# Kernel tuning notes

Hardware: AMD Instinct MI355X
Metric: run time of the kernel (lower is better)

Reference implementation:

```python
import jax, jax.numpy as jnp
import numpy as np

B, S, H = 1, 4096, 2048
NH, NKV, HD = 16, 4, 128  # query heads, kv heads, head_dim
THETA = 1000000.0
NEG = -1e9


def setup_inputs() -> dict:
    key = jax.random.key(0)
    ks = jax.random.split(key, 5)
    hidden_states = jax.random.normal(ks[0], (B, S, H), jnp.float32) * 0.02
    Wq = jax.random.normal(ks[1], (H, NH * HD), jnp.float32) * 0.02
    Wk = jax.random.normal(ks[2], (H, NKV * HD), jnp.float32) * 0.02
    Wv = jax.random.normal(ks[3], (H, NKV * HD), jnp.float32) * 0.02
    Wo = jax.random.normal(ks[4], (H, H), jnp.float32) * 0.02
    # additive causal mask [B,1,S,S]
    causal = jnp.tril(jnp.ones((S, S), bool))
    attention_mask = jnp.where(causal, 0.0, NEG).astype(jnp.float32)[None, None]
    position_ids = jnp.arange(S, dtype=jnp.int32)[None]
    return dict(hidden_states=hidden_states, Wq=Wq, Wk=Wk, Wv=Wv, Wo=Wo,
                attention_mask=attention_mask, position_ids=position_ids)


def _rotate_half(x):
    return jnp.concatenate([-x[..., HD // 2:], x[..., :HD // 2]], axis=-1)


def reference(hidden_states, Wq, Wk, Wv, Wo, attention_mask, position_ids):
    # projections -> [B, heads, S, HD]
    q = (hidden_states @ Wq).reshape(B, S, NH, HD).transpose(0, 2, 1, 3)
    k = (hidden_states @ Wk).reshape(B, S, NKV, HD).transpose(0, 2, 1, 3)
    v = (hidden_states @ Wv).reshape(B, S, NKV, HD).transpose(0, 2, 1, 3)

    # RoPE (HF style: freqs duplicated across halves, rotate_half)
    inv_freq = 1.0 / (THETA ** (jnp.arange(0, HD, 2, dtype=jnp.float32) / HD))
    freqs = position_ids.astype(jnp.float32)[..., None] * inv_freq  # [B,S,HD/2]
    emb = jnp.concatenate([freqs, freqs], axis=-1)                  # [B,S,HD]
    cos = jnp.cos(emb)[:, None].astype(q.dtype)                     # [B,1,S,HD]
    sin = jnp.sin(emb)[:, None].astype(q.dtype)
    q = q * cos + _rotate_half(q) * sin
    k = k * cos + _rotate_half(k) * sin

    # GQA: repeat each kv head consecutively (matches torch repeat_kv)
    rep = NH // NKV
    k = jnp.repeat(k, rep, axis=1)
    v = jnp.repeat(v, rep, axis=1)

    scale = 1.0 / jnp.sqrt(jnp.float32(HD))
    scores = jnp.einsum('bhqd,bhkd->bhqk', q, k) * scale + attention_mask
    attn = jax.nn.softmax(scores.astype(jnp.float32), axis=-1).astype(q.dtype)
    out = jnp.einsum('bhqk,bhkd->bhqd', attn, v)  # [B,NH,S,HD]
    out = out.transpose(0, 2, 1, 3).reshape(B, S, H)
    return out @ Wo
```

## Files before the change

kernel.cpp:

```cpp
#include <hip/hip_runtime.h>
#include <stdint.h>

typedef uint16_t u16;
typedef __bf16  bf16x8 __attribute__((ext_vector_type(8)));
typedef float   f32x4  __attribute__((ext_vector_type(4)));
typedef float   f32x16 __attribute__((ext_vector_type(16)));
typedef uint16_t u16x8 __attribute__((ext_vector_type(8), may_alias));
typedef uint32_t u32x4 __attribute__((ext_vector_type(4)));

typedef const __attribute__((address_space(1))) void* gas_p;
typedef __attribute__((address_space(3))) void* las_p;

#define SCALE2 0.1275430214486847f

__device__ __forceinline__ void load_lds16(const void* g, void* l) {
    __builtin_amdgcn_global_load_lds((gas_p)g, (las_p)l, 16, 0, 0);
}

__device__ __forceinline__ u16 f2bf(float f) {
    uint32_t u = __builtin_bit_cast(uint32_t, f);
    u += 0x7FFFu + ((u >> 16) & 1u);
    return (u16)(u >> 16);
}
__device__ __forceinline__ float bf2f(u16 h) {
    uint32_t u = ((uint32_t)h) << 16;
    return __builtin_bit_cast(float, u);
}
__device__ __forceinline__ bf16x8 ld_frag(const u16* p) {
    u16x8 t = *(const u16x8*)p;
    return __builtin_bit_cast(bf16x8, t);
}
__device__ __forceinline__ uint32_t cvt_pk_bf16(float lo, float hi) {
    uint32_t r;
    asm("v_cvt_pk_bf16_f32 %0, %1, %2" : "=v"(r) : "v"(lo), "v"(hi));
    return r;
}
__device__ __forceinline__ void plane32_swap(uint32_t& a, uint32_t& b) {
    asm("v_permlane32_swap_b32 %0, %1" : "+v"(a), "+v"(b));
}

__global__ __launch_bounds__(256) void prep(const float* __restrict__ hidden,
                                            u16* __restrict__ Hb,
                                            const float* __restrict__ Wq,
                                            u16* __restrict__ WqT,
                                            const float* __restrict__ Wk,
                                            const float* __restrict__ Wv,
                                            u16* __restrict__ WkvT) {
    __shared__ u16 tile[64][65];
    const int bid = blockIdx.x;
    const int tx  = threadIdx.x;
    if (bid < 4096) {
        int i = bid * 256 + tx;
        const float* p = hidden + (size_t)i * 8;
        u16x8 o;
#pragma unroll
        for (int j = 0; j < 8; j++) o[j] = f2bf(p[j]);
        *(u16x8*)(Hb + (size_t)i * 8) = o;
        return;
    }
    const float* in;
    u16* out;
    int R, C, bx, by;
    if (bid < 5120)      { int l = bid - 4096; in = Wq; out = WqT;            R = 2048; C = 2048; bx = l & 31; by = l >> 5; }
    else if (bid < 5376) { int l = bid - 5120; in = Wk; out = WkvT;           R = 2048; C = 512;  bx = l & 7;  by = l >> 3; }
    else                 { int l = bid - 5376; in = Wv; out = WkvT + 1048576; R = 2048; C = 512;  bx = l & 7;  by = l >> 3; }
    const int bc = bx * 64, br = by * 64;
#pragma unroll
    for (int i = 0; i < 16; i++) {
        int idx = tx + i * 256;
        int r = idx >> 6, c = idx & 63;
        tile[r][c] = f2bf(in[(size_t)(br + r) * C + bc + c]);
    }
    __syncthreads();
#pragma unroll
    for (int i = 0; i < 16; i++) {
        int idx = tx + i * 256;
        int r = idx >> 6, c = idx & 63;
        out[(size_t)(bc + r) * R + br + c] = tile[c][r];
    }
}

__global__ __launch_bounds__(256) void mid(u16* __restrict__ Q,
                                           u16* __restrict__ KV,
                                           const float* __restrict__ Wo,
                                           u16* __restrict__ WoT,
                                           u16* __restrict__ VT) {
    __shared__ u16 tile[64][65];
    const int bid = blockIdx.x;
    const int tx  = threadIdx.x;
    if (bid < 20480) {
        int g = bid * 256 + tx;
        int d = g & 63;
        int row = g >> 6;
        int s = row / 20;
        int hh = row - s * 20;
        u16* buf = (hh < 16) ? (Q + (size_t)s * 2048 + hh * 128)
                             : (KV + (size_t)s * 1024 + (hh - 16) * 128);
        float p = (float)s;
        float angle = p * exp2f((float)d * (-19.931568569324174f / 64.0f));
        float sc = (hh < 16) ? SCALE2 : 1.0f;
        float c = cosf(angle) * sc, sn = sinf(angle) * sc;
        float x0 = bf2f(buf[d]), x1 = bf2f(buf[d + 64]);
        buf[d]      = f2bf(x0 * c - x1 * sn);
        buf[d + 64] = f2bf(x1 * c + x0 * sn);
        return;
    }
    if (bid < 21504) {
        int l = bid - 20480;
        int bc = (l & 31) * 64, br = (l >> 5) * 64;
#pragma unroll
        for (int i = 0; i < 16; i++) {
            int idx = tx + i * 256;
            int r = idx >> 6, c = idx & 63;
            tile[r][c] = f2bf(Wo[(size_t)(br + r) * 2048 + bc + c]);
        }
        __syncthreads();
#pragma unroll
        for (int i = 0; i < 16; i++) {
            int idx = tx + i * 256;
            int r = idx >> 6, c = idx & 63;
            WoT[(size_t)(bc + r) * 2048 + br + c] = tile[c][r];
        }
        return;
    }
    {
        int l = bid - 21504;
        int bc = (l & 7) * 64, br = (l >> 3) * 64;
#pragma unroll
        for (int i = 0; i < 16; i++) {
            int idx = tx + i * 256;
            int r = idx >> 6, c = idx & 63;
            tile[r][c] = KV[(size_t)(br + r) * 1024 + 512 + bc + c];
        }
        __syncthreads();
#pragma unroll
        for (int i = 0; i < 16; i++) {
            int idx = tx + i * 256;
            int r = idx >> 6, c = idx & 63;
            VT[(size_t)(bc + r) * 4096 + br + c] = tile[c][r];
        }
    }
}

#define TM 128
#define TN 128

__global__ __launch_bounds__(256) void gemm_qkv(const u16* __restrict__ A,
                                                const u16* __restrict__ WqT,
                                                const u16* __restrict__ WkvT,
                                                u16* __restrict__ Qb,
                                                u16* __restrict__ KVb) {
    __shared__ u16 As[128 * 64];
    __shared__ u16 Bs[128 * 64];
    const int K = 2048;
    const int tid  = threadIdx.x;
    const int wave = tid >> 6;
    const int lane = tid & 63;
    const int l15  = lane & 15;
    const int quad = lane >> 4;
    const int m0 = blockIdx.y * TM;
    const int n0 = blockIdx.x * TN;
    const u16* Bt;
    u16* C;
    int ldC, cbase;
    if (n0 < 2048) { Bt = WqT + (size_t)n0 * K;          C = Qb;  ldC = 2048; cbase = n0; }
    else           { Bt = WkvT + (size_t)(n0 - 2048) * K; C = KVb; ldC = 1024; cbase = n0 - 2048; }
    const int wm = (wave >> 1) * 64;
    const int wn = (wave & 1) * 64;

    f32x4 acc[4][4] = {};

    const int srow = tid >> 3;
    const int swc  = ((tid & 7) ^ (srow & 7)) * 8;
    const u16* Ap[4];
    const u16* Bp[4];
#pragma unroll
    for (int r = 0; r < 4; r++) {
        Ap[r] = A  + (size_t)(m0 + srow + r * 32) * K + swc;
        Bp[r] = Bt + (size_t)(srow + r * 32) * K + swc;
    }
    u16* AsD = As + wave * 512;
    u16* BsD = Bs + wave * 512;

    for (int k0 = 0; k0 < K; k0 += 64) {
#pragma unroll
        for (int r = 0; r < 4; r++) load_lds16(Ap[r] + k0, AsD + r * 2048);
#pragma unroll
        for (int r = 0; r < 4; r++) load_lds16(Bp[r] + k0, BsD + r * 2048);
        __syncthreads();
        bf16x8 af[2][4], bfr[2][4];
        const int sx = (l15 & 7) << 3;
#pragma unroll
        for (int kk = 0; kk < 2; kk++)
#pragma unroll
            for (int i = 0; i < 4; i++) {
                af[kk][i]  = ld_frag(&As[((wm + i * 16 + l15) * 64 + kk * 32 + quad * 8) ^ sx]);
                bfr[kk][i] = ld_frag(&Bs[((wn + i * 16 + l15) * 64 + kk * 32 + quad * 8) ^ sx]);
            }
#pragma unroll
        for (int kk = 0; kk < 2; kk++)
#pragma unroll
            for (int i = 0; i < 4; i++)
#pragma unroll
                for (int j = 0; j < 4; j++)
                    acc[i][j] = __builtin_amdgcn_mfma_f32_16x16x32_bf16(af[kk][i], bfr[kk][j], acc[i][j], 0, 0, 0);
        __syncthreads();
    }
#pragma unroll
    for (int i = 0; i < 4; i++)
#pragma unroll
        for (int j = 0; j < 4; j++)
#pragma unroll
            for (int r = 0; r < 4; r++) {
                int row = m0 + wm + i * 16 + quad * 4 + r;
                int col = cbase + wn + j * 16 + l15;
                C[(size_t)row * ldC + col] = f2bf(acc[i][j][r]);
            }
}

template <bool F32OUT>
__global__ __launch_bounds__(256) void gemm_bt(const u16* __restrict__ A,
                                               const u16* __restrict__ Bt,
                                               void* __restrict__ Cp,
                                               int M, int N, int K) {
    __shared__ u16 As[128 * 64];
    __shared__ u16 Bs[128 * 64];
    const int tid  = threadIdx.x;
    const int wave = tid >> 6;
    const int lane = tid & 63;
    const int l15  = lane & 15;
    const int quad = lane >> 4;
    const int m0 = blockIdx.y * TM;
    const int n0 = blockIdx.x * TN;
    const int wm = (wave >> 1) * 64;
    const int wn = (wave & 1) * 64;

    f32x4 acc[4][4] = {};

    const int srow = tid >> 3;
    const int swc  = ((tid & 7) ^ (srow & 7)) * 8;
    const u16* Ap[4];
    const u16* Bp[4];
#pragma unroll
    for (int r = 0; r < 4; r++) {
        Ap[r] = A  + (size_t)(m0 + srow + r * 32) * K + swc;
        Bp[r] = Bt + (size_t)(n0 + srow + r * 32) * K + swc;
    }
    u16* AsD = As + wave * 512;
    u16* BsD = Bs + wave * 512;

    for (int k0 = 0; k0 < K; k0 += 64) {
#pragma unroll
        for (int r = 0; r < 4; r++) load_lds16(Ap[r] + k0, AsD + r * 2048);
#pragma unroll
        for (int r = 0; r < 4; r++) load_lds16(Bp[r] + k0, BsD + r * 2048);
        __syncthreads();
        bf16x8 af[2][4], bfr[2][4];
        const int sx = (l15 & 7) << 3;
#pragma unroll
        for (int kk = 0; kk < 2; kk++)
#pragma unroll
            for (int i = 0; i < 4; i++) {
                af[kk][i]  = ld_frag(&As[((wm + i * 16 + l15) * 64 + kk * 32 + quad * 8) ^ sx]);
                bfr[kk][i] = ld_frag(&Bs[((wn + i * 16 + l15) * 64 + kk * 32 + quad * 8) ^ sx]);
            }
#pragma unroll
        for (int kk = 0; kk < 2; kk++)
#pragma unroll
            for (int i = 0; i < 4; i++)
#pragma unroll
                for (int j = 0; j < 4; j++)
                    acc[i][j] = __builtin_amdgcn_mfma_f32_16x16x32_bf16(af[kk][i], bfr[kk][j], acc[i][j], 0, 0, 0);
        __syncthreads();
    }
#pragma unroll
    for (int i = 0; i < 4; i++)
#pragma unroll
        for (int j = 0; j < 4; j++)
#pragma unroll
            for (int r = 0; r < 4; r++) {
                int row = m0 + wm + i * 16 + quad * 4 + r;
                int col = n0 + wn + j * 16 + l15;
                if (F32OUT)
                    ((float*)Cp)[(size_t)row * N + col] = acc[i][j][r];
                else
                    ((u16*)Cp)[(size_t)row * N + col] = f2bf(acc[i][j][r]);
            }
}

#define QK1(CC, MSK)                                                           \
  do {                                                                         \
    const int krow_ = (CC) * 32 + l31;                                         \
    f32x16 sv_ = {};                                                           \
    _Pragma("unroll")                                                          \
    for (int dk = 0; dk < 8; dk++) {                                           \
      bf16x8 kf = ld_frag(&Kb[krow_ * 128 + (((dk * 2 + hi8) + krow_) & 15) * 8]); \
      sv_ = __builtin_amdgcn_mfma_f32_32x32x16_bf16(kf, qf[dk], sv_, 0, 0, 0); \
    }                                                                          \
    float p_[16]; float rs_ = 0.f;                                             \
    const int kvbs_ = kv0 + (CC) * 32 + 4 * hi8;                               \
    _Pragma("unroll")                                                          \
    for (int r = 0; r < 16; r++) {                                             \
      float pe = exp2f(sv_[r]);                                                \
      if (MSK) { int kvv = kvbs_ + (r & 3) + 8 * (r >> 2);                     \
                 pe = (kvv <= qrow) ? pe : 0.f; }                              \
      p_[r] = pe; rs_ += pe;                                                   \
    }                                                                          \
    lr += rs_;                                                                 \
    uint32_t w0 = cvt_pk_bf16(p_[0], p_[1]);                                   \
    uint32_t w1 = cvt_pk_bf16(p_[2], p_[3]);                                   \
    uint32_t w2 = cvt_pk_bf16(p_[4], p_[5]);                                   \
    uint32_t w3 = cvt_pk_bf16(p_[6], p_[7]);                                   \
    plane32_swap(w0, w2); plane32_swap(w1, w3);                                \
    uint32_t w4 = cvt_pk_bf16(p_[8], p_[9]);                                   \
    uint32_t w5 = cvt_pk_bf16(p_[10], p_[11]);                                 \
    uint32_t w6 = cvt_pk_bf16(p_[12], p_[13]);                                 \
    plane32_swap(w4, w6);                                                      \
    uint32_t w7 = cvt_pk_bf16(p_[14], p_[15]);                                 \
    plane32_swap(w5, w7);                                                      \
    u32x4 a0_ = {w0, w1, w2, w3}, a1_ = {w4, w5, w6, w7};                      \
    bf16x8 pa0_ = __builtin_bit_cast(bf16x8, a0_);                             \
    bf16x8 pa1_ = __builtin_bit_cast(bf16x8, a1_);                             \
    _Pragma("unroll")                                                          \
    for (int ks2 = 0; ks2 < 2; ks2++) {                                        \
      bf16x8 pa_ = ks2 ? pa1_ : pa0_;                                          \
      _Pragma("unroll")                                                        \
      for (int nt = 0; nt < 4; nt++) {                                         \
        const int d_ = nt * 32 + l31;                                          \
        bf16x8 vf = ld_frag(&Vb[d_ * 64 + ((((CC) * 4 + ks2 * 2 + hi8) + d_) & 7) * 8]); \
        acc[nt] = __builtin_amdgcn_mfma_f32_32x32x16_bf16(pa_, vf, acc[nt], 0, 0, 0); \
      }                                                                        \
    }                                                                          \
  } while (0)

__global__ __launch_bounds__(256, 2) void flash_attn9(const u16* __restrict__ Q,
                                                      const u16* __restrict__ KVb,
                                                      const u16* __restrict__ VT,
                                                      u16* __restrict__ Op0,
                                                      u16* __restrict__ Op1,
                                                      float* __restrict__ Lp) {
    __shared__ u16 Ks[2][8192];
    __shared__ u16 Vs[2][8192];
    const int tid  = threadIdx.x;
    const int ww   = tid >> 6;
    const int lane = tid & 63;
    const int l31  = lane & 31;
    const int hi8  = lane >> 5;
    const int bid  = blockIdx.x;
    const int h    = (bid & 7) * 2 + ((bid >> 3) & 1);
    const int rest = bid >> 4;
    const int j    = 31 - (rest >> 1);
    const int s    = rest & 1;
    const int kvh  = h >> 2;
    const int qg0  = j * 128 + ww * 32;
    const int qrow = qg0 + l31;
    const int dW   = qg0 >> 6;
    const int kb0  = s * (j + 1);
    const int kb1  = kb0 + (j + 1);

    bf16x8 qf[8];
    {
        const u16* qp = Q + (size_t)qrow * 2048 + h * 128 + hi8 * 8;
#pragma unroll
        for (int dk = 0; dk < 8; dk++) qf[dk] = ld_frag(qp + dk * 16);
    }

    const u16* srcK[4];
    const u16* srcV[4];
#pragma unroll
    for (int r = 0; r < 4; r++) {
        int p = r * 256 + tid;
        int kv = p >> 4;
        srcK[r] = KVb + (size_t)kv * 1024 + kvh * 128 + ((((p & 15) - kv) & 15) * 8);
        int d = p >> 3;
        srcV[r] = VT + (size_t)(kvh * 128 + d) * 4096 + ((((p & 7) - (d & 7)) & 7) * 8);
    }

    f32x16 acc[4] = {};
    float lr = 0.f;

#pragma unroll
    for (int r = 0; r < 4; r++) {
        load_lds16(srcK[r] + (size_t)(kb0 * 64) * 1024, &Ks[0][r * 2048 + ww * 512]);
        load_lds16(srcV[r] + kb0 * 64, &Vs[0][r * 2048 + ww * 512]);
    }
    asm volatile("s_waitcnt vmcnt(0)" ::: "memory");
    __syncthreads();

    for (int kvb = kb0; kvb < kb1; kvb++) {
        const int cur = (kvb - kb0) & 1;
        if (kvb + 1 < kb1) {
            const int kvn = (kvb + 1) * 64;
#pragma unroll
            for (int r = 0; r < 4; r++) {
                load_lds16(srcK[r] + (size_t)kvn * 1024, &Ks[cur ^ 1][r * 2048 + ww * 512]);
                load_lds16(srcV[r] + kvn, &Vs[cur ^ 1][r * 2048 + ww * 512]);
            }
        }
        const u16* Kb = Ks[cur];
        const u16* Vb = Vs[cur];
        const int kv0 = kvb * 64;

        if (kvb < dW) {
            QK1(0, 0);
            QK1(1, 0);
        } else if (kvb == dW) {
            QK1(0, 1);
            QK1(1, 1);
        }

        asm volatile("s_waitcnt vmcnt(0)" ::: "memory");
        __syncthreads();
    }

    float lt = lr + __shfl_xor(lr, 32);
    if (lane < 32) Lp[(s * 16 + h) * 4096 + qg0 + l31] = lt;
    u16* Ops = s ? Op1 : Op0;
#pragma unroll
    for (int r = 0; r < 16; r++) {
        int qr = (r & 3) + 8 * (r >> 2) + 4 * hi8;
        u16* op = Ops + (size_t)(qg0 + qr) * 2048 + h * 128 + l31;
#pragma unroll
        for (int nt = 0; nt < 4; nt++)
            op[nt * 32] = f2bf(acc[nt][r]);
    }
}

__global__ __launch_bounds__(256) void merge_o(u16* __restrict__ o0,
                                               const u16* __restrict__ o1,
                                               const float* __restrict__ Lp) {
    int i = blockIdx.x * 256 + threadIdx.x;
    size_t base = (size_t)i * 8;
    int row = (int)(base >> 11);
    int h   = (int)((base >> 7) & 15);
    float inv = 1.0f / (Lp[h * 4096 + row] + Lp[(16 + h) * 4096 + row]);
    u16x8 a = *(const u16x8*)(o0 + base);
    u16x8 b = *(const u16x8*)(o1 + base);
    u16x8 o;
#pragma unroll
    for (int jj = 0; jj < 8; jj++)
        o[jj] = f2bf((bf2f(a[jj]) + bf2f(b[jj])) * inv);
    *(u16x8*)(o0 + base) = o;
}

__global__ __launch_bounds__(256, 2) void flash_attn7(const u16* __restrict__ Q,
                                                      const u16* __restrict__ KVb,
                                                      const u16* __restrict__ VT,
                                                      u16* __restrict__ O) {
    __shared__ u16 Ks[2][8192];
    __shared__ u16 Vs[2][8192];
    __shared__ float Llds[4][32];
    const int tid  = threadIdx.x;
    const int ww   = tid >> 6;
    const int lane = tid & 63;
    const int l31  = lane & 31;
    const int hi8  = lane >> 5;
    const int bid  = blockIdx.x;
    const int h    = bid >> 5;
    const int cls  = bid & 31;
    const int bx   = cls >> 1;
    const int z    = cls & 1;
    const int kvh  = h >> 2;
    const int qt0  = z ? (3968 - bx * 128) : (bx * 128);
    const int qg0  = qt0 + ww * 32;
    const int qrow = qg0 + l31;
    const int dW   = qg0 >> 6;
    const int nkv  = (qt0 >> 6) + 2;

    bf16x8 qf[8];
    {
        const u16* qp = Q + (size_t)qrow * 2048 + h * 128 + hi8 * 8;
#pragma unroll
        for (int dk = 0; dk < 8; dk++) qf[dk] = ld_frag(qp + dk * 16);
    }

    const u16* srcK[4];
    const u16* srcV[4];
#pragma unroll
    for (int r = 0; r < 4; r++) {
        int p = r * 256 + tid;
        int kv = p >> 4;
        srcK[r] = KVb + (size_t)kv * 1024 + kvh * 128 + ((((p & 15) - kv) & 15) * 8);
        int d = p >> 3;
        srcV[r] = VT + (size_t)(kvh * 128 + d) * 4096 + ((((p & 7) - (d & 7)) & 7) * 8);
    }

    f32x16 acc[4] = {};
    float lr = 0.f;

#pragma unroll
    for (int r = 0; r < 4; r++) {
        load_lds16(srcK[r], &Ks[0][r * 2048 + ww * 512]);
        load_lds16(srcV[r], &Vs[0][r * 2048 + ww * 512]);
    }
    asm volatile("s_waitcnt vmcnt(0)" ::: "memory");
    __syncthreads();

    for (int kvb = 0; kvb < nkv; kvb++) {
        const int cur = kvb & 1;
        if (kvb + 1 < nkv) {
            const int kvn = (kvb + 1) * 64;
#pragma unroll
            for (int r = 0; r < 4; r++) {
                load_lds16(srcK[r] + (size_t)kvn * 1024, &Ks[cur ^ 1][r * 2048 + ww * 512]);
                load_lds16(srcV[r] + kvn, &Vs[cur ^ 1][r * 2048 + ww * 512]);
            }
        }
        const u16* Kb = Ks[cur];
        const u16* Vb = Vs[cur];
        const int kv0 = kvb * 64;

        if (kvb < dW) {
            QK1(0, 0);
            QK1(1, 0);
        } else if (kvb == dW) {
            QK1(0, 1);
            QK1(1, 1);
        }

        asm volatile("s_waitcnt vmcnt(0)" ::: "memory");
        __syncthreads();
    }

    float lt = lr + __shfl_xor(lr, 32);
    if (lane < 32) Llds[ww][l31] = lt;
    __syncthreads();
#pragma unroll
    for (int r = 0; r < 16; r++) {
        int qr = (r & 3) + 8 * (r >> 2) + 4 * hi8;
        float linv = 1.0f / Llds[ww][qr];
        u16* op = O + (size_t)(qg0 + qr) * 2048 + h * 128 + l31;
#pragma unroll
        for (int nt = 0; nt < 4; nt++)
            op[nt * 32] = f2bf(acc[nt][r] * linv);
    }
}

extern "C" void kernel_launch(void* const* d_in, const int* in_sizes, int n_in,
                              void* d_out, int out_size, void* d_ws, size_t ws_size,
                              hipStream_t stream) {
    const float* hidden = (const float*)d_in[0];
    const float* Wq = (const float*)d_in[1];
    const float* Wk = (const float*)d_in[2];
    const float* Wv = (const float*)d_in[3];
    const float* Wo = (const float*)d_in[4];
    float* out = (float*)d_out;

    u16* ws   = (u16*)d_ws;
    u16* Hb   = ws;
    u16* Qb   = Hb   + 8388608;
    u16* KVb  = Qb   + 8388608;
    u16* WqT  = KVb  + 4194304;
    u16* WkvT = WqT  + 4194304;
    u16* VT   = WkvT + 2097152;
    u16* Op1  = VT   + 4194304;
    const size_t WS_SPLIT = (size_t)(31457280 + 8388608) * 2;

    prep<<<dim3(5632), 256, 0, stream>>>(hidden, Hb, Wq, WqT, Wk, Wv, WkvT);

    gemm_qkv<<<dim3(24, 32), 256, 0, stream>>>(Hb, WqT, WkvT, Qb, KVb);

    u16* WoT = WqT;
    mid<<<dim3(22016), 256, 0, stream>>>(Qb, KVb, Wo, WoT, VT);

    u16* Ob = Hb;
    if (ws_size >= WS_SPLIT) {
        float* Lp = (float*)WkvT;
        flash_attn9<<<dim3(1024), 256, 0, stream>>>(Qb, KVb, VT, Ob, Op1, Lp);
        merge_o<<<dim3(4096), 256, 0, stream>>>(Ob, Op1, Lp);
    } else {
        flash_attn7<<<dim3(512), 256, 0, stream>>>(Qb, KVb, VT, Ob);
    }

    gemm_bt<true><<<dim3(16, 32), 256, 0, stream>>>(Ob, WoT, out, 4096, 2048, 2048);
}
```

Before: 379.5 us.

## Compute softmax row sums via MFMA with ones vector and unroll double-buffer loop

Replaces the per-lane scalar row-sum accumulation of exponentials with an extra MFMA against a bf16 ones vector, so the denominator comes out of the matrix unit and needs no final shuffle. Both 32-key QK/softmax chunks are now computed before the PV MFMAs, and the KV loop is unrolled by two so buffer indices are compile-time constants. The sum is now taken over bf16-rounded probabilities, which matches the numerator but changes rounding, and the extra MFMAs and live P fragments add compute and register pressure.

```diff
diff --git a/kernel.cpp b/kernel.cpp
--- a/kernel.cpp
+++ b/kernel.cpp
@@ -288,6 +288,55 @@
             }
 }
 
+#define QKSM(CC, MSK, PA)                                                      \
+  do {                                                                         \
+    const int krow_ = (CC) * 32 + l31;                                         \
+    f32x16 sv_ = {};                                                           \
+    _Pragma("unroll")                                                          \
+    for (int dk = 0; dk < 8; dk++) {                                           \
+      bf16x8 kf = ld_frag(&Kb[krow_ * 128 + (((dk * 2 + hi8) + krow_) & 15) * 8]); \
+      sv_ = __builtin_amdgcn_mfma_f32_32x32x16_bf16(kf, qf[dk], sv_, 0, 0, 0); \
+    }                                                                          \
+    float p_[16];                                                              \
+    const int kvbs_ = kv0 + (CC) * 32 + 4 * hi8;                               \
+    _Pragma("unroll")                                                          \
+    for (int r = 0; r < 16; r++) {                                             \
+      float pe = exp2f(sv_[r]);                                                \
+      if (MSK) { int kvv = kvbs_ + (r & 3) + 8 * (r >> 2);                     \
+                 pe = (kvv <= qrow) ? pe : 0.f; }                              \
+      p_[r] = pe;                                                              \
+    }                                                                          \
+    uint32_t w0 = cvt_pk_bf16(p_[0], p_[1]);                                   \
+    uint32_t w1 = cvt_pk_bf16(p_[2], p_[3]);                                   \
+    uint32_t w2 = cvt_pk_bf16(p_[4], p_[5]);                                   \
+    uint32_t w3 = cvt_pk_bf16(p_[6], p_[7]);                                   \
+    plane32_swap(w0, w2); plane32_swap(w1, w3);                                \
+    uint32_t w4 = cvt_pk_bf16(p_[8], p_[9]);                                   \
+    uint32_t w5 = cvt_pk_bf16(p_[10], p_[11]);                                 \
+    uint32_t w6 = cvt_pk_bf16(p_[12], p_[13]);                                 \
+    plane32_swap(w4, w6);                                                      \
+    uint32_t w7 = cvt_pk_bf16(p_[14], p_[15]);                                 \
+    plane32_swap(w5, w7);                                                      \
+    u32x4 a0_ = {w0, w1, w2, w3}, a1_ = {w4, w5, w6, w7};                      \
+    PA[0] = __builtin_bit_cast(bf16x8, a0_);                                   \
+    PA[1] = __builtin_bit_cast(bf16x8, a1_);                                   \
+  } while (0)
+
+#define PVL(CC, PA)                                                            \
+  do {                                                                         \
+    _Pragma("unroll")                                                          \
+    for (int ks2 = 0; ks2 < 2; ks2++) {                                        \
+      bf16x8 pa_ = PA[ks2];                                                    \
+      _Pragma("unroll")                                                        \
+      for (int nt = 0; nt < 4; nt++) {                                         \
+        const int d_ = nt * 32 + l31;                                          \
+        bf16x8 vf = ld_frag(&Vb[d_ * 64 + ((((CC) * 4 + ks2 * 2 + hi8) + d_) & 7) * 8]); \
+        acc[nt] = __builtin_amdgcn_mfma_f32_32x32x16_bf16(pa_, vf, acc[nt], 0, 0, 0); \
+      }                                                                        \
+      accL = __builtin_amdgcn_mfma_f32_32x32x16_bf16(pa_, onesf, accL, 0, 0, 0); \
+    }                                                                          \
+  } while (0)
+
 #define QK1(CC, MSK)                                                           \
   do {                                                                         \
     const int krow_ = (CC) * 32 + l31;                                         \
@@ -333,12 +382,38 @@
     }                                                                          \
   } while (0)
 
-__global__ __launch_bounds__(256, 2) void flash_attn9(const u16* __restrict__ Q,
-                                                      const u16* __restrict__ KVb,
-                                                      const u16* __restrict__ VT,
-                                                      u16* __restrict__ Op0,
-                                                      u16* __restrict__ Op1,
-                                                      float* __restrict__ Lp) {
+#define FA_BODY(B, T)                                                          \
+  do {                                                                         \
+    const bool pre_ = ((T) + 1 < nloc);                                        \
+    if (pre_) {                                                                \
+        const int kvn_ = (kb0 + (T) + 1) * 64;                                 \
+        _Pragma("unroll")                                                      \
+        for (int r = 0; r < 4; r++) {                                          \
+            load_lds16(srcK[r] + (size_t)kvn_ * 1024, &Ks[(B) ^ 1][r * 2048 + ww * 512]); \
+            load_lds16(srcV[r] + kvn_, &Vs[(B) ^ 1][r * 2048 + ww * 512]);     \
+        }                                                                      \
+    }                                                                          \
+    const u16* Kb = Ks[B];                                                     \
+    const u16* Vb = Vs[B];                                                     \
+    const int kvb = kb0 + (T);                                                 \
+    const int kv0 = kvb * 64;                                                  \
+    if (kvb <= dW) {                                                           \
+        bf16x8 pa0[2], pa1[2];                                                 \
+        if (kvb == dW) { QKSM(0, 1, pa0); QKSM(1, 1, pa1); }                   \
+        else           { QKSM(0, 0, pa0); QKSM(1, 0, pa1); }                   \
+        PVL(0, pa0);                                                           \
+        PVL(1, pa1);                                                           \
+    }                                                                          \
+    asm volatile("s_waitcnt vmcnt(0)" ::: "memory");                           \
+    __syncthreads();                                                           \
+  } while (0)
+
+__global__ __launch_bounds__(256, 2) void flash_attn11(const u16* __restrict__ Q,
+                                                       const u16* __restrict__ KVb,
+                                                       const u16* __restrict__ VT,
+                                                       u16* __restrict__ Op0,
+                                                       u16* __restrict__ Op1,
+                                                       float* __restrict__ Lp) {
     __shared__ u16 Ks[2][8192];
     __shared__ u16 Vs[2][8192];
     const int tid  = threadIdx.x;
@@ -356,7 +431,7 @@
     const int qrow = qg0 + l31;
     const int dW   = qg0 >> 6;
     const int kb0  = s * (j + 1);
-    const int kb1  = kb0 + (j + 1);
+    const int nloc = j + 1;
 
     bf16x8 qf[8];
     {
@@ -377,7 +452,9 @@
     }
 
     f32x16 acc[4] = {};
-    float lr = 0.f;
+    f32x16 accL = {};
+    const u32x4 onesw = {0x3F803F80u, 0x3F803F80u, 0x3F803F80u, 0x3F803F80u};
+    const bf16x8 onesf = __builtin_bit_cast(bf16x8, onesw);
 
 #pragma unroll
     for (int r = 0; r < 4; r++) {
@@ -387,34 +464,18 @@
     asm volatile("s_waitcnt vmcnt(0)" ::: "memory");
     __syncthreads();
 
-    for (int kvb = kb0; kvb < kb1; kvb++) {
-        const int cur = (kvb - kb0) & 1;
-        if (kvb + 1 < kb1) {
-            const int kvn = (kvb + 1) * 64;
-#pragma unroll
-            for (int r = 0; r < 4; r++) {
-                load_lds16(srcK[r] + (size_t)kvn * 1024, &Ks[cur ^ 1][r * 2048 + ww * 512]);
-                load_lds16(srcV[r] + kvn, &Vs[cur ^ 1][r * 2048 + ww * 512]);
-            }
+    for (int tt = 0; tt < nloc; tt += 2) {
+        FA_BODY(0, tt);
+        if (tt + 1 < nloc) FA_BODY(1, tt + 1);
+    }
+
+    if (l31 == 0) {
+#pragma unroll
+        for (int r = 0; r < 16; r++) {
+            int q = (r & 3) + 8 * (r >> 2) + 4 * hi8;
+            Lp[(s * 16 + h) * 4096 + qg0 + q] = accL[r];
         }
-        const u16* Kb = Ks[cur];
-        const u16* Vb = Vs[cur];
-        const int kv0 = kvb * 64;
-
-        if (kvb < dW) {
-            QK1(0, 0);
-            QK1(1, 0);
-        } else if (kvb == dW) {
-            QK1(0, 1);
-            QK1(1, 1);
-        }
-
-        asm volatile("s_waitcnt vmcnt(0)" ::: "memory");
-        __syncthreads();
-    }
-
-    float lt = lr + __shfl_xor(lr, 32);
-    if (lane < 32) Lp[(s * 16 + h) * 4096 + qg0 + l31] = lt;
+    }
     u16* Ops = s ? Op1 : Op0;
 #pragma unroll
     for (int r = 0; r < 16; r++) {
@@ -566,7 +627,7 @@
     u16* Ob = Hb;
     if (ws_size >= WS_SPLIT) {
         float* Lp = (float*)WkvT;
-        flash_attn9<<<dim3(1024), 256, 0, stream>>>(Qb, KVb, VT, Ob, Op1, Lp);
+        flash_attn11<<<dim3(1024), 256, 0, stream>>>(Qb, KVb, VT, Ob, Op1, Lp);
         merge_o<<<dim3(4096), 256, 0, stream>>>(Ob, Op1, Lp);
     } else {
         flash_attn7<<<dim3(512), 256, 0, stream>>>(Qb, KVb, VT, Ob);
```

New measurement: 383.0 us. No clear change (+0.9%).
